# Kernel optimization log

Hardware: AMD Instinct MI355X
Metric: run time of the kernel (lower is better)

## Reference

```python
import jax, jax.numpy as jnp
import numpy as np

ID, IH, IW = 8, 16, 16
HEADS, DIM_HEAD = 8, 32
INP, OUP = 256, 256
B = 4
N = ID * IH * IW  # 2048
INNER = HEADS * DIM_HEAD  # 256
SCALE = DIM_HEAD ** -0.5


def _make_relative_pos():
    # Faithful to the torch ctor: 3D coords, pairwise diffs, linearize, shift to >=0
    z, y, x = np.meshgrid(np.arange(ID), np.arange(IH), np.arange(IW), indexing='ij')
    coords = np.stack([z.ravel(), y.ravel(), x.ravel()], axis=1)  # [N,3]
    rel = coords[:, None, :] - coords[None, :, :]                 # [N,N,3]
    rp = rel[:, :, 0] * (IH * IW) + rel[:, :, 1] * IW + rel[:, :, 2]
    rp = rp - rp.min()
    return jnp.asarray(rp, dtype=jnp.int32)                       # [N,N]


def setup_inputs() -> dict:
    key = jax.random.key(0)
    k1, k2, k3, k4, k5 = jax.random.split(key, 5)
    table_size = ID * IH * IW * 8  # 16384, as in nn.Embedding ctor
    return {
        "x": jax.random.normal(k1, (B, N, INP), dtype=jnp.float32),
        "w_qkv": jax.random.normal(k2, (INP, 3 * INNER), dtype=jnp.float32) * (INP ** -0.5),
        "bias_table": jax.random.normal(k3, (table_size, 1), dtype=jnp.float32),
        "w_out": jax.random.normal(k4, (INNER, OUP), dtype=jnp.float32) * (INNER ** -0.5),
        "b_out": jax.random.normal(k5, (OUP,), dtype=jnp.float32),
        "relative_pos": _make_relative_pos(),
    }


def reference(x, w_qkv, bias_table, w_out, b_out, relative_pos):
    Bb, Nn, C = x.shape
    qkv = x @ w_qkv                                   # [B, N, 3*H*D]
    qkv = qkv.reshape(Bb, Nn, 3, HEADS, DIM_HEAD)
    qkv = jnp.transpose(qkv, (2, 0, 3, 1, 4))         # [3, B, H, N, D]
    q, k, v = qkv[0], qkv[1], qkv[2]
    q = q * SCALE
    attn = jnp.einsum('bhnd,bhmd->bhnm', q, k)        # [B, H, N, N]
    bias = bias_table[relative_pos, 0]                # [N, N], shared across B,H
    attn = attn + bias
    attn = jax.nn.softmax(attn, axis=-1)
    out = jnp.einsum('bhnm,bhmd->bhnd', attn, v)      # [B, H, N, D]
    out = jnp.transpose(out, (0, 2, 1, 3)).reshape(Bb, Nn, INNER)
    return out @ w_out + b_out                        # dropout p=0 -> identity
```

## Files before the change

### kernel.cpp

```cpp
#include <hip/hip_runtime.h>

typedef unsigned short u16;
typedef unsigned int u32;
typedef __attribute__((ext_vector_type(8))) short bf16x8;
typedef __attribute__((ext_vector_type(4))) float f32x4;

#define MFMA16(a, b, c) __builtin_amdgcn_mfma_f32_16x16x32_bf16(a, b, c, 0, 0, 0)

__device__ __forceinline__ float hw_exp2(float x) { return __builtin_amdgcn_exp2f(x); }

__device__ __forceinline__ u16 f2bf(float f) {
    union { float f; u32 i; } v; v.f = f;
    u32 x = v.i;
    return (u16)((x + 0x7FFFu + ((x >> 16) & 1u)) >> 16);
}

__global__ __launch_bounds__(256) void k_prep(const float* __restrict__ x,
                                              const float* __restrict__ wqkv,
                                              const float* __restrict__ wout,
                                              u16* __restrict__ xb,
                                              u16* __restrict__ wqkvT,
                                              u16* __restrict__ woutT) {
    const float QSCALE2 = 0.2550566756538019f;
    int bx = blockIdx.x, tid = threadIdx.x;
    if (bx < 1024) {
        int base = bx * 2048 + tid * 8;
        float4 a = *(const float4*)(x + base);
        float4 b = *(const float4*)(x + base + 4);
        uint4 r;
        r.x = f2bf(a.x) | ((u32)f2bf(a.y) << 16);
        r.y = f2bf(a.z) | ((u32)f2bf(a.w) << 16);
        r.z = f2bf(b.x) | ((u32)f2bf(b.y) << 16);
        r.w = f2bf(b.z) | ((u32)f2bf(b.w) << 16);
        *(uint4*)(xb + base) = r;
    } else if (bx < 1792) {
        int idx = (bx - 1024) * 256 + tid;
        int n = idx >> 8, kk = idx & 255;
        float sc = (n < 256) ? QSCALE2 : 1.0f;
        wqkvT[idx] = f2bf(wqkv[kk * 768 + n] * sc);
    } else {
        int idx = (bx - 1792) * 256 + tid;
        int n = idx >> 8, kk = idx & 255;
        woutT[idx] = f2bf(wout[kk * 256 + n]);
    }
}

__global__ __launch_bounds__(256) void k_gemm_qkv(const u16* __restrict__ xb,
                                                  const u16* __restrict__ wT,
                                                  u16* __restrict__ qkv) {
    const int tid = threadIdx.x;
    const int wave = tid >> 6, lane = tid & 63, quad = lane >> 4, ql = lane & 15;
    const int mbase = blockIdx.x * 128 + (wave & 1) * 64;
    const int nbase = blockIdx.y * 64 + (wave >> 1) * 32;
    f32x4 acc[4][2];
#pragma unroll
    for (int i = 0; i < 4; ++i)
#pragma unroll
        for (int j = 0; j < 2; ++j) acc[i][j] = (f32x4){0.f, 0.f, 0.f, 0.f};
#pragma unroll
    for (int ks = 0; ks < 8; ++ks) {
        bf16x8 af[4], bfm[2];
#pragma unroll
        for (int ms = 0; ms < 4; ++ms)
            af[ms] = *(const bf16x8*)(xb + (size_t)(mbase + ms * 16 + ql) * 256 + ks * 32 + quad * 8);
#pragma unroll
        for (int ns = 0; ns < 2; ++ns)
            bfm[ns] = *(const bf16x8*)(wT + (size_t)(nbase + ns * 16 + ql) * 256 + ks * 32 + quad * 8);
#pragma unroll
        for (int ms = 0; ms < 4; ++ms)
#pragma unroll
            for (int ns = 0; ns < 2; ++ns)
                acc[ms][ns] = MFMA16(af[ms], bfm[ns], acc[ms][ns]);
    }
#pragma unroll
    for (int ms = 0; ms < 4; ++ms)
#pragma unroll
        for (int ns = 0; ns < 2; ++ns) {
            int colb = nbase + ns * 16;
            int t = colb >> 8;
            int Mrow0 = mbase + ms * 16 + quad * 4;
            int bb = Mrow0 >> 11, nn0 = Mrow0 & 2047;
            int col = colb + ql;
            int h = (col & 255) >> 5, d = col & 31;
            if (t == 2) {
                u16 e0 = f2bf(acc[ms][ns][0]), e1 = f2bf(acc[ms][ns][1]);
                u16 e2 = f2bf(acc[ms][ns][2]), e3 = f2bf(acc[ms][ns][3]);
                uint2 pp; pp.x = e0 | ((u32)e1 << 16); pp.y = e2 | ((u32)e3 << 16);
                *(uint2*)(qkv + (size_t)2 * 2097152 + (size_t)(bb * 8 + h) * 65536 +
                          (size_t)d * 2048 + nn0) = pp;
            } else {
#pragma unroll
                for (int r = 0; r < 4; ++r)
                    qkv[(size_t)t * 2097152 + ((size_t)(bb * 8 + h) * 2048 + nn0 + r) * 32 + d] =
                        f2bf(acc[ms][ns][r]);
            }
        }
}

__global__ __launch_bounds__(256, 4) void k_attn(const u16* __restrict__ q,
                                                 const u16* __restrict__ k,
                                                 const u16* __restrict__ vT,
                                                 const float* __restrict__ table,
                                                 u16* __restrict__ att) {
    __shared__ __align__(16) u16 kbuf[2][2048];
    __shared__ __align__(16) u16 vbuf[2][2048];
    __shared__ float tbl2[2112];
    __shared__ u32 pT[4][640];
    const int tid = threadIdx.x;
    const int bh = blockIdx.x & 31, qt = blockIdx.x >> 5;
    const int wave = tid >> 6, lane = tid & 63, quad = lane >> 4, ql = lane & 15;
    const float LOG2E = 1.4426950408889634f;

    const u16* kbh = k + (size_t)bh * 65536;
    const u16* vbh = vT + (size_t)bh * 65536;

    const u16* kgbase = kbh + wave * 512 + lane * 8;
    const int vd = wave * 8 + (lane >> 3);
    const u16* vgbase = vbh + (size_t)vd * 2048 + (((lane & 7) ^ (vd & 7)) << 3);

#define DMA(BUF, KT) do {                                                               \
    __builtin_amdgcn_global_load_lds(                                                   \
        (const __attribute__((address_space(1))) void*)(kgbase + (KT) * 2048),          \
        (__attribute__((address_space(3))) void*)(&kbuf[BUF][wave * 512]), 16, 0, 0);   \
    __builtin_amdgcn_global_load_lds(                                                   \
        (const __attribute__((address_space(1))) void*)(vgbase + (KT) * 64),            \
        (__attribute__((address_space(3))) void*)(&vbuf[BUF][wave * 512]), 16, 0, 0);   \
} while (0)

    DMA(0, 0);

    const float4* tg = (const float4*)(table + qt * 64);
    for (int i = tid; i < 528; i += 256) {
        float4 t = tg[i];
        t.x *= LOG2E; t.y *= LOG2E; t.z *= LOG2E; t.w *= LOG2E;
        ((float4*)tbl2)[i] = t;
    }

    const int qr0 = qt * 64 + wave * 16 + ql;
    const bf16x8 qf = *(const bf16x8*)(q + ((size_t)bh * 2048 + qr0) * 32 + quad * 8);
    const int bloc = wave * 16 + ql + 2047 - quad * 4;

    bf16x8 ones;
#pragma unroll
    for (int i = 0; i < 8; ++i) ones[i] = (short)0x3F80;

    f32x4 oT0 = {0.f, 0.f, 0.f, 0.f}, oT1 = {0.f, 0.f, 0.f, 0.f}, oL = {0.f, 0.f, 0.f, 0.f};
    u32* pw = &pT[wave][0];

    __syncthreads();

    for (int kt = 0; kt < 32; ++kt) {
        const int buf = kt & 1;
        if (kt < 31) DMA(buf ^ 1, kt + 1);

        const u16* kb = &kbuf[buf][0];
        const u16* vb = &vbuf[buf][0];
        bf16x8 kf[4], vf[4];
#pragma unroll
        for (int j = 0; j < 4; ++j)
            kf[j] = *(const bf16x8*)(kb + (j * 16 + ql) * 32 + quad * 8);
#pragma unroll
        for (int f = 0; f < 4; ++f) {
            int c = f >> 1, dt = f & 1;
            vf[f] = *(const bf16x8*)(vb + (dt * 16 + ql) * 64 + (((c * 4 + quad) ^ (ql & 7)) << 3));
        }

        f32x4 z = {0.f, 0.f, 0.f, 0.f};
        f32x4 s[4];
#pragma unroll
        for (int j = 0; j < 4; ++j) s[j] = MFMA16(kf[j], qf, z);
#pragma unroll
        for (int j = 0; j < 4; ++j)
#pragma unroll
            for (int r = 0; r < 4; ++r)
                s[j][r] = hw_exp2(s[j][r] + tbl2[bloc - kt * 64 - j * 16 - r]);
#pragma unroll
        for (int j = 0; j < 4; ++j)
#pragma unroll
            for (int p = 0; p < 2; ++p)
                pw[(j * 8 + quad * 2 + p) * 20 + ql] = __builtin_amdgcn_perm(
                    __float_as_uint(s[j][2 * p + 1]), __float_as_uint(s[j][2 * p]),
                    0x07060302u);
#pragma unroll
        for (int c = 0; c < 2; ++c) {
            union { u32 u[4]; bf16x8 v; } bb;
#pragma unroll
            for (int kk = 0; kk < 4; ++kk)
                bb.u[kk] = pw[(c * 16 + quad * 4 + kk) * 20 + ql];
            oT0 = MFMA16(vf[c * 2 + 0], bb.v, oT0);
            oT1 = MFMA16(vf[c * 2 + 1], bb.v, oT1);
            oL  = MFMA16(ones, bb.v, oL);
        }
        __syncthreads();
    }
#undef DMA

    float inv = 1.0f / oL[0];
    size_t base = ((size_t)bh * 2048 + qr0) * 32;
#pragma unroll
    for (int dt = 0; dt < 2; ++dt) {
        u16 e0 = f2bf(oT0[0] * inv), e1 = f2bf(oT0[1] * inv);
        u16 e2 = f2bf(oT0[2] * inv), e3 = f2bf(oT0[3] * inv);
        if (dt == 1) {
            e0 = f2bf(oT1[0] * inv); e1 = f2bf(oT1[1] * inv);
            e2 = f2bf(oT1[2] * inv); e3 = f2bf(oT1[3] * inv);
        }
        uint2 pp; pp.x = e0 | ((u32)e1 << 16); pp.y = e2 | ((u32)e3 << 16);
        *(uint2*)(att + base + dt * 16 + quad * 4) = pp;
    }
}

__global__ __launch_bounds__(256) void k_gemm_out(const u16* __restrict__ attq,
                                                  const u16* __restrict__ wT,
                                                  const float* __restrict__ bout,
                                                  float* __restrict__ out) {
    const int tid = threadIdx.x;
    const int wave = tid >> 6, lane = tid & 63, quad = lane >> 4, ql = lane & 15;
    const int mbase = blockIdx.x * 128 + (wave & 1) * 64;
    const int nbase = blockIdx.y * 64 + (wave >> 1) * 32;
    f32x4 acc[4][2];
#pragma unroll
    for (int i = 0; i < 4; ++i)
#pragma unroll
        for (int j = 0; j < 2; ++j) acc[i][j] = (f32x4){0.f, 0.f, 0.f, 0.f};
#pragma unroll
    for (int ks = 0; ks < 8; ++ks) {
        bf16x8 af[4], bfm[2];
#pragma unroll
        for (int ms = 0; ms < 4; ++ms) {
            int row = mbase + ms * 16 + ql;
            af[ms] = *(const bf16x8*)(attq +
                ((size_t)((row >> 11) * 8 + ks) * 2048 + (row & 2047)) * 32 + quad * 8);
        }
#pragma unroll
        for (int ns = 0; ns < 2; ++ns)
            bfm[ns] = *(const bf16x8*)(wT + (size_t)(nbase + ns * 16 + ql) * 256 + ks * 32 + quad * 8);
#pragma unroll
        for (int ms = 0; ms < 4; ++ms)
#pragma unroll
            for (int ns = 0; ns < 2; ++ns)
                acc[ms][ns] = MFMA16(af[ms], bfm[ns], acc[ms][ns]);
    }
#pragma unroll
    for (int ms = 0; ms < 4; ++ms)
#pragma unroll
        for (int ns = 0; ns < 2; ++ns)
#pragma unroll
            for (int r = 0; r < 4; ++r) {
                int Mrow = mbase + ms * 16 + quad * 4 + r;
                int col = nbase + ns * 16 + ql;
                out[(size_t)Mrow * 256 + col] = acc[ms][ns][r] + bout[col];
            }
}

extern "C" void kernel_launch(void* const* d_in, const int* in_sizes, int n_in,
                              void* d_out, int out_size, void* d_ws, size_t ws_size,
                              hipStream_t stream) {
    const float* x    = (const float*)d_in[0];
    const float* wqkv = (const float*)d_in[1];
    const float* btab = (const float*)d_in[2];
    const float* wout = (const float*)d_in[3];
    const float* bout = (const float*)d_in[4];
    float* out = (float*)d_out;

    if (ws_size < (size_t)13107200) return;
    u16* ws = (u16*)d_ws;
    u16* wqkvT = ws;
    u16* woutT = wqkvT + 196608;
    u16* qkv   = woutT + 65536;
    u16* xb    = (u16*)d_out;

    hipLaunchKernelGGL(k_prep, dim3(2048), dim3(256), 0, stream, x, wqkv, wout, xb, wqkvT, woutT);
    hipLaunchKernelGGL(k_gemm_qkv, dim3(64, 12), dim3(256), 0, stream, xb, wqkvT, qkv);
    hipLaunchKernelGGL(k_attn, dim3(1024), dim3(256), 0, stream,
                       qkv, qkv + 2097152, qkv + 2 * 2097152, btab, qkv);
    hipLaunchKernelGGL(k_gemm_out, dim3(64, 4), dim3(256), 0, stream, qkv, woutT, bout, out);
}
```

Before: 149.4 us.

## Process two key tiles per barrier and vectorize P staging in attention

The attention loop now loads two 64-key tiles per DMA stage, so it runs 16 iterations with half as many __syncthreads. The K tile layout in LDS is XOR-swizzled to cut bank conflicts. The P transpose buffer is reorganized so each lane writes with a 64-bit store and reads back with a single 128-bit load, replacing scalar accesses. Shared memory use roughly doubles for K/V, and launch bounds drop from 4 to 3 blocks per SM, which may lower occupancy.

```diff
diff --git a/kernel.cpp b/kernel.cpp
--- a/kernel.cpp
+++ b/kernel.cpp
@@ -97,15 +97,15 @@
         }
 }
 
-__global__ __launch_bounds__(256, 4) void k_attn(const u16* __restrict__ q,
+__global__ __launch_bounds__(256, 3) void k_attn(const u16* __restrict__ q,
                                                  const u16* __restrict__ k,
                                                  const u16* __restrict__ vT,
                                                  const float* __restrict__ table,
                                                  u16* __restrict__ att) {
-    __shared__ __align__(16) u16 kbuf[2][2048];
-    __shared__ __align__(16) u16 vbuf[2][2048];
+    __shared__ __align__(16) u16 kbuf[2][2][2048];
+    __shared__ __align__(16) u16 vbuf[2][2][2048];
     __shared__ float tbl2[2112];
-    __shared__ u32 pT[4][640];
+    __shared__ u32 pT[4][16 * 36];
     const int tid = threadIdx.x;
     const int bh = blockIdx.x & 31, qt = blockIdx.x >> 5;
     const int wave = tid >> 6, lane = tid & 63, quad = lane >> 4, ql = lane & 15;
@@ -114,17 +114,19 @@
     const u16* kbh = k + (size_t)bh * 65536;
     const u16* vbh = vT + (size_t)bh * 65536;
 
-    const u16* kgbase = kbh + wave * 512 + lane * 8;
+    const int krow = wave * 16 + (lane >> 2);
+    const u16* kg = kbh + krow * 32 + ((((lane & 3) ^ ((lane >> 3) & 3))) << 3);
     const int vd = wave * 8 + (lane >> 3);
-    const u16* vgbase = vbh + (size_t)vd * 2048 + (((lane & 7) ^ (vd & 7)) << 3);
-
-#define DMA(BUF, KT) do {                                                               \
-    __builtin_amdgcn_global_load_lds(                                                   \
-        (const __attribute__((address_space(1))) void*)(kgbase + (KT) * 2048),          \
-        (__attribute__((address_space(3))) void*)(&kbuf[BUF][wave * 512]), 16, 0, 0);   \
-    __builtin_amdgcn_global_load_lds(                                                   \
-        (const __attribute__((address_space(1))) void*)(vgbase + (KT) * 64),            \
-        (__attribute__((address_space(3))) void*)(&vbuf[BUF][wave * 512]), 16, 0, 0);   \
+    const u16* vg = vbh + (size_t)vd * 2048 + (((lane & 7) ^ (vd & 7)) << 3);
+
+#define GLDS(SRC, DST) __builtin_amdgcn_global_load_lds(                         \
+        (const __attribute__((address_space(1))) void*)(SRC),                    \
+        (__attribute__((address_space(3))) void*)(DST), 16, 0, 0)
+#define DMA(BUF, PAIR) do {                                                      \
+    GLDS(kg + (PAIR) * 4096,        &kbuf[BUF][0][wave * 512]);                  \
+    GLDS(kg + (PAIR) * 4096 + 2048, &kbuf[BUF][1][wave * 512]);                  \
+    GLDS(vg + (PAIR) * 128,         &vbuf[BUF][0][wave * 512]);                  \
+    GLDS(vg + (PAIR) * 128 + 64,    &vbuf[BUF][1][wave * 512]);                  \
 } while (0)
 
     DMA(0, 0);
@@ -139,6 +141,8 @@
     const int qr0 = qt * 64 + wave * 16 + ql;
     const bf16x8 qf = *(const bf16x8*)(q + ((size_t)bh * 2048 + qr0) * 32 + quad * 8);
     const int bloc = wave * 16 + ql + 2047 - quad * 4;
+    const int kro = ((quad ^ ((ql >> 1) & 3)) << 3);
+    const int pbase = ql * 36;
 
     bf16x8 ones;
 #pragma unroll
@@ -149,51 +153,56 @@
 
     __syncthreads();
 
-    for (int kt = 0; kt < 32; ++kt) {
-        const int buf = kt & 1;
-        if (kt < 31) DMA(buf ^ 1, kt + 1);
-
-        const u16* kb = &kbuf[buf][0];
-        const u16* vb = &vbuf[buf][0];
-        bf16x8 kf[4], vf[4];
-#pragma unroll
-        for (int j = 0; j < 4; ++j)
-            kf[j] = *(const bf16x8*)(kb + (j * 16 + ql) * 32 + quad * 8);
-#pragma unroll
-        for (int f = 0; f < 4; ++f) {
-            int c = f >> 1, dt = f & 1;
-            vf[f] = *(const bf16x8*)(vb + (dt * 16 + ql) * 64 + (((c * 4 + quad) ^ (ql & 7)) << 3));
-        }
-
-        f32x4 z = {0.f, 0.f, 0.f, 0.f};
-        f32x4 s[4];
-#pragma unroll
-        for (int j = 0; j < 4; ++j) s[j] = MFMA16(kf[j], qf, z);
-#pragma unroll
-        for (int j = 0; j < 4; ++j)
-#pragma unroll
-            for (int r = 0; r < 4; ++r)
-                s[j][r] = hw_exp2(s[j][r] + tbl2[bloc - kt * 64 - j * 16 - r]);
-#pragma unroll
-        for (int j = 0; j < 4; ++j)
-#pragma unroll
-            for (int p = 0; p < 2; ++p)
-                pw[(j * 8 + quad * 2 + p) * 20 + ql] = __builtin_amdgcn_perm(
-                    __float_as_uint(s[j][2 * p + 1]), __float_as_uint(s[j][2 * p]),
-                    0x07060302u);
-#pragma unroll
-        for (int c = 0; c < 2; ++c) {
-            union { u32 u[4]; bf16x8 v; } bb;
-#pragma unroll
-            for (int kk = 0; kk < 4; ++kk)
-                bb.u[kk] = pw[(c * 16 + quad * 4 + kk) * 20 + ql];
-            oT0 = MFMA16(vf[c * 2 + 0], bb.v, oT0);
-            oT1 = MFMA16(vf[c * 2 + 1], bb.v, oT1);
-            oL  = MFMA16(ones, bb.v, oL);
+    for (int pr = 0; pr < 16; ++pr) {
+        const int buf = pr & 1;
+        if (pr < 15) DMA(buf ^ 1, pr + 1);
+
+#pragma unroll
+        for (int t = 0; t < 2; ++t) {
+            const int kt = pr * 2 + t;
+            const u16* kb = &kbuf[buf][t][0];
+            const u16* vb = &vbuf[buf][t][0];
+            bf16x8 kf[4], vf[4];
+#pragma unroll
+            for (int j = 0; j < 4; ++j)
+                kf[j] = *(const bf16x8*)(kb + (j * 16 + ql) * 32 + kro);
+#pragma unroll
+            for (int f = 0; f < 4; ++f) {
+                int c = f >> 1, dt = f & 1;
+                vf[f] = *(const bf16x8*)(vb + (dt * 16 + ql) * 64 +
+                                         (((c * 4 + quad) ^ (ql & 7)) << 3));
+            }
+
+            f32x4 z = {0.f, 0.f, 0.f, 0.f};
+            f32x4 s[4];
+#pragma unroll
+            for (int j = 0; j < 4; ++j) s[j] = MFMA16(kf[j], qf, z);
+#pragma unroll
+            for (int j = 0; j < 4; ++j)
+#pragma unroll
+                for (int r = 0; r < 4; ++r)
+                    s[j][r] = hw_exp2(s[j][r] + tbl2[bloc - kt * 64 - j * 16 - r]);
+#pragma unroll
+            for (int j = 0; j < 4; ++j) {
+                uint2 w;
+                w.x = __builtin_amdgcn_perm(__float_as_uint(s[j][1]),
+                                            __float_as_uint(s[j][0]), 0x07060302u);
+                w.y = __builtin_amdgcn_perm(__float_as_uint(s[j][3]),
+                                            __float_as_uint(s[j][2]), 0x07060302u);
+                *(uint2*)&pw[pbase + j * 8 + quad * 2] = w;
+            }
+#pragma unroll
+            for (int c = 0; c < 2; ++c) {
+                bf16x8 pa = *(const bf16x8*)&pw[pbase + c * 16 + quad * 4];
+                oT0 = MFMA16(vf[c * 2 + 0], pa, oT0);
+                oT1 = MFMA16(vf[c * 2 + 1], pa, oT1);
+                oL  = MFMA16(ones, pa, oL);
+            }
         }
         __syncthreads();
     }
 #undef DMA
+#undef GLDS
 
     float inv = 1.0f / oL[0];
     size_t base = ((size_t)bh * 2048 + qr0) * 32;
```

Result: no change. 147.9 us (-1.0%).
